# Performance work log

Measured on AMD Instinct MI355X. Metric: run time of the kernel, lower is better.

## Reference

```python
import jax, jax.numpy as jnp
import numpy as np

D_IN, D_H1, D_H2, D_OUT = 24, 64, 128, 64

def setup_inputs() -> dict:
    key = jax.random.key(0)
    ks = jax.random.split(key, 7)
    B, L = 256, 2048
    input_data = jax.random.normal(ks[0], (B, L, D_IN), dtype=jnp.float32)
    s = lambda fan_in: 1.0 / np.sqrt(fan_in)
    W1 = jax.random.uniform(ks[1], (D_IN, D_H1), minval=-s(D_IN), maxval=s(D_IN), dtype=jnp.float32)
    b1 = jax.random.uniform(ks[2], (D_H1,), minval=-s(D_IN), maxval=s(D_IN), dtype=jnp.float32)
    W2 = jax.random.uniform(ks[3], (D_H1, D_H2), minval=-s(D_H1), maxval=s(D_H1), dtype=jnp.float32)
    b2 = jax.random.uniform(ks[4], (D_H2,), minval=-s(D_H1), maxval=s(D_H1), dtype=jnp.float32)
    W3 = jax.random.uniform(ks[5], (D_H2, D_OUT), minval=-s(D_H2), maxval=s(D_H2), dtype=jnp.float32)
    b3 = jax.random.uniform(ks[6], (D_OUT,), minval=-s(D_H2), maxval=s(D_H2), dtype=jnp.float32)
    return {"input_data": input_data, "W1": W1, "b1": b1, "W2": W2, "b2": b2, "W3": W3, "b3": b3, "batch_size": 256}

def reference(input_data, W1, b1, W2, b2, W3, b3, batch_size):
    # Vectorized equivalent of the per-(batch,line) MLP loop:
    # three Linear+ReLU layers applied to every [24]-dim vector.
    h = jax.nn.relu(jnp.einsum('bli,ij->blj', input_data, W1) + b1)
    h = jax.nn.relu(jnp.einsum('bli,ij->blj', h, W2) + b2)
    out = jax.nn.relu(jnp.einsum('bli,ij->blj', h, W3) + b3)  # [B, L, 64]
    return out
```

## Files before the change

kernel.cpp:

```cpp
#include <hip/hip_runtime.h>

typedef float f32x4 __attribute__((ext_vector_type(4)));
typedef short s16x8 __attribute__((ext_vector_type(8)));

#define DIN 24
#define DH1 64
#define DH2 128
#define DOUT 64
#define H1PAD 80
#define H2PAD 136

static __device__ __forceinline__ unsigned short f2bf(float f) {
    unsigned int u = __builtin_bit_cast(unsigned int, f);
    u += 0x7FFFu + ((u >> 16) & 1u);
    return (unsigned short)(u >> 16);
}

__global__ __launch_bounds__(256, 2) void linenet_mfma(
    const float* __restrict__ in,
    const float* __restrict__ W1, const float* __restrict__ b1,
    const float* __restrict__ W2, const float* __restrict__ b2,
    const float* __restrict__ W3, const float* __restrict__ b3,
    float* __restrict__ out, int M)
{
    __shared__ __align__(16) unsigned short w3lds[16 * 64 * 8];
    __shared__ __align__(16) unsigned short h1lds[4][16 * H1PAD];
    __shared__ __align__(16) unsigned short h2lds[4][16 * H2PAD];

    const int tid = threadIdx.x;

    for (int it = tid; it < 16 * 64; it += 256) {
        const int frag = it >> 6;
        const int ln   = it & 63;
        const int ks   = frag >> 2, nt = frag & 3;
        const int g    = ln >> 4,   c  = ln & 15;
        #pragma unroll
        for (int j = 0; j < 8; ++j) {
            const int k = 32 * ks + 8 * g + j;
            w3lds[it * 8 + j] = f2bf(W3[k * DOUT + nt * 16 + c]);
        }
    }
    __syncthreads();

    const int wave = tid >> 6, lane = tid & 63;
    const int gl = lane >> 4, cl = lane & 15;

    s16x8 w1f[4];
    #pragma unroll
    for (int nt = 0; nt < 4; ++nt) {
        #pragma unroll
        for (int j = 0; j < 8; ++j) {
            const int k = 8 * gl + j;
            w1f[nt][j] = (k < DIN) ? (short)f2bf(W1[k * DH1 + nt * 16 + cl]) : (short)0;
        }
    }
    s16x8 w2f[2][8];
    #pragma unroll
    for (int ks = 0; ks < 2; ++ks)
        #pragma unroll
        for (int nt = 0; nt < 8; ++nt)
            #pragma unroll
            for (int j = 0; j < 8; ++j)
                w2f[ks][nt][j] = (short)f2bf(W2[(32 * ks + 8 * gl + j) * DH2 + nt * 16 + cl]);

    float b1v[4], b2v[8], b3v[4];
    #pragma unroll
    for (int nt = 0; nt < 4; ++nt) b1v[nt] = b1[nt * 16 + cl];
    #pragma unroll
    for (int nt = 0; nt < 8; ++nt) b2v[nt] = b2[nt * 16 + cl];
    #pragma unroll
    for (int nt = 0; nt < 4; ++nt) b3v[nt] = b3[nt * 16 + cl];

    unsigned short* const h1p = &h1lds[wave][0];
    unsigned short* const h2p = &h2lds[wave][0];

    const int NT = M / 16;
    const int nw = (int)gridDim.x * 4;
    int t = (int)blockIdx.x * 4 + wave;
    if (t >= NT) return;

    const int goff = (gl < 3) ? 8 * gl : 16;
    const int loff = cl * DIN + goff;

    f32x4 pf0, pf1;
    {
        const float* p = in + (size_t)t * (16 * DIN) + loff;
        pf0 = *(const f32x4*)p;
        pf1 = *(const f32x4*)(p + 4);
    }

    f32x4 zac = {0.f, 0.f, 0.f, 0.f};

    while (t < NT) {
        s16x8 a1;
        #pragma unroll
        for (int j = 0; j < 4; ++j) {
            a1[j]     = (short)f2bf(pf0[j]);
            a1[4 + j] = (short)f2bf(pf1[j]);
        }

        const int tn = t + nw;
        {
            const int tc = (tn < NT) ? tn : t;
            const float* p = in + (size_t)tc * (16 * DIN) + loff;
            pf0 = *(const f32x4*)p;
            pf1 = *(const f32x4*)(p + 4);
        }

        f32x4 acc1[4];
        #pragma unroll
        for (int nt = 0; nt < 4; ++nt)
            acc1[nt] = __builtin_amdgcn_mfma_f32_16x16x32_bf16(a1, w1f[nt], zac, 0, 0, 0);

        #pragma unroll
        for (int nt = 0; nt < 4; ++nt)
            #pragma unroll
            for (int r = 0; r < 4; ++r) {
                float v = fmaxf(acc1[nt][r] + b1v[nt], 0.f);
                h1p[(4 * gl + r) * H1PAD + nt * 16 + cl] = f2bf(v);
            }

        s16x8 a2[2];
        #pragma unroll
        for (int ks = 0; ks < 2; ++ks)
            a2[ks] = *(const s16x8*)&h1p[cl * H1PAD + 32 * ks + 8 * gl];

        f32x4 acc2[8];
        #pragma unroll
        for (int nt = 0; nt < 8; ++nt)
            acc2[nt] = __builtin_amdgcn_mfma_f32_16x16x32_bf16(a2[0], w2f[0][nt], zac, 0, 0, 0);
        #pragma unroll
        for (int nt = 0; nt < 8; ++nt)
            acc2[nt] = __builtin_amdgcn_mfma_f32_16x16x32_bf16(a2[1], w2f[1][nt], acc2[nt], 0, 0, 0);

        #pragma unroll
        for (int nt = 0; nt < 8; ++nt)
            #pragma unroll
            for (int r = 0; r < 4; ++r) {
                float v = fmaxf(acc2[nt][r] + b2v[nt], 0.f);
                h2p[(4 * gl + r) * H2PAD + nt * 16 + cl] = f2bf(v);
            }

        f32x4 acc3[4];
        #pragma unroll
        for (int ks = 0; ks < 4; ++ks) {
            const s16x8 a3 = *(const s16x8*)&h2p[cl * H2PAD + 32 * ks + 8 * gl];
            #pragma unroll
            for (int nt = 0; nt < 4; ++nt) {
                const s16x8 wf = *(const s16x8*)&w3lds[((ks * 4 + nt) * 64 + lane) * 8];
                acc3[nt] = __builtin_amdgcn_mfma_f32_16x16x32_bf16(
                    a3, wf, (ks == 0) ? zac : acc3[nt], 0, 0, 0);
            }
        }

        float* const ob = out + (size_t)t * (16 * DOUT);
        #pragma unroll
        for (int nt = 0; nt < 4; ++nt)
            #pragma unroll
            for (int r = 0; r < 4; ++r) {
                float v = fmaxf(acc3[nt][r] + b3v[nt], 0.f);
                ob[(4 * gl + r) * DOUT + nt * 16 + cl] = v;
            }

        t = tn;
    }
}

extern "C" void kernel_launch(void* const* d_in, const int* in_sizes, int n_in,
                              void* d_out, int out_size, void* d_ws, size_t ws_size,
                              hipStream_t stream)
{
    const float* in = (const float*)d_in[0];
    const float* W1 = (const float*)d_in[1];
    const float* b1 = (const float*)d_in[2];
    const float* W2 = (const float*)d_in[3];
    const float* b2 = (const float*)d_in[4];
    const float* W3 = (const float*)d_in[5];
    const float* b3 = (const float*)d_in[6];
    float* out = (float*)d_out;
    const int M = in_sizes[0] / DIN;

    dim3 grid(512), block(256);
    hipLaunchKernelGGL(linenet_mfma, grid, block, 0, stream,
                       in, W1, b1, W2, b2, W3, b3, out, M);
}
```

Baseline: 49.92 us.

## Transpose MFMA operands so outputs are row-contiguous, fold bias into layer one

Swaps the MFMA operand order so each lane's accumulator holds four consecutive output features of one row. This allows packed bf16 stores to LDS via v_cvt_pk_bf16_f32 and 16-byte vector global stores instead of scalar scattered writes. The layer-1 bias is folded into the matmul by placing a constant 1.0 in the padded K slot. W3 fragments now live in registers instead of LDS, which raises register pressure under the 2-wave-per-SIMD launch bound.

```diff
diff --git a/kernel.cpp b/kernel.cpp
--- a/kernel.cpp
+++ b/kernel.cpp
@@ -2,74 +2,76 @@
 
 typedef float f32x4 __attribute__((ext_vector_type(4)));
 typedef short s16x8 __attribute__((ext_vector_type(8)));
+typedef unsigned int u32;
 
 #define DIN 24
 #define DH1 64
 #define DH2 128
 #define DOUT 64
-#define H1PAD 80
-#define H2PAD 136
+#define S1 72
+#define S2 136
 
 static __device__ __forceinline__ unsigned short f2bf(float f) {
-    unsigned int u = __builtin_bit_cast(unsigned int, f);
+    u32 u = __builtin_bit_cast(u32, f);
     u += 0x7FFFu + ((u >> 16) & 1u);
     return (unsigned short)(u >> 16);
 }
 
-__global__ __launch_bounds__(256, 2) void linenet_mfma(
+static __device__ __forceinline__ u32 cvtpk(float lo, float hi) {
+    u32 r;
+    asm("v_cvt_pk_bf16_f32 %0, %1, %2" : "=v"(r) : "v"(lo), "v"(hi));
+    return r;
+}
+
+__global__ __launch_bounds__(256, 2) void linenet_mfma_t(
     const float* __restrict__ in,
     const float* __restrict__ W1, const float* __restrict__ b1,
     const float* __restrict__ W2, const float* __restrict__ b2,
     const float* __restrict__ W3, const float* __restrict__ b3,
     float* __restrict__ out, int M)
 {
-    __shared__ __align__(16) unsigned short w3lds[16 * 64 * 8];
-    __shared__ __align__(16) unsigned short h1lds[4][16 * H1PAD];
-    __shared__ __align__(16) unsigned short h2lds[4][16 * H2PAD];
+    __shared__ __align__(16) unsigned short h1lds[4][1152];
+    __shared__ __align__(16) unsigned short h2lds[4][2176];
 
-    const int tid = threadIdx.x;
-
-    for (int it = tid; it < 16 * 64; it += 256) {
-        const int frag = it >> 6;
-        const int ln   = it & 63;
-        const int ks   = frag >> 2, nt = frag & 3;
-        const int g    = ln >> 4,   c  = ln & 15;
-        #pragma unroll
-        for (int j = 0; j < 8; ++j) {
-            const int k = 32 * ks + 8 * g + j;
-            w3lds[it * 8 + j] = f2bf(W3[k * DOUT + nt * 16 + c]);
-        }
-    }
-    __syncthreads();
-
+    const int tid  = threadIdx.x;
     const int wave = tid >> 6, lane = tid & 63;
     const int gl = lane >> 4, cl = lane & 15;
 
-    s16x8 w1f[4];
+    s16x8 w1tf[4];
     #pragma unroll
-    for (int nt = 0; nt < 4; ++nt) {
+    for (int nt = 0; nt < 4; ++nt)
         #pragma unroll
         for (int j = 0; j < 8; ++j) {
             const int k = 8 * gl + j;
-            w1f[nt][j] = (k < DIN) ? (short)f2bf(W1[k * DH1 + nt * 16 + cl]) : (short)0;
+            unsigned short v = 0;
+            if (k < DIN)       v = f2bf(W1[k * DH1 + nt * 16 + cl]);
+            else if (k == DIN) v = f2bf(b1[nt * 16 + cl]);
+            w1tf[nt][j] = (short)v;
         }
-    }
-    s16x8 w2f[2][8];
+    s16x8 w2tf[8][2];
     #pragma unroll
-    for (int ks = 0; ks < 2; ++ks)
+    for (int mt = 0; mt < 8; ++mt)
         #pragma unroll
-        for (int nt = 0; nt < 8; ++nt)
+        for (int ks = 0; ks < 2; ++ks)
             #pragma unroll
             for (int j = 0; j < 8; ++j)
-                w2f[ks][nt][j] = (short)f2bf(W2[(32 * ks + 8 * gl + j) * DH2 + nt * 16 + cl]);
+                w2tf[mt][ks][j] =
+                    (short)f2bf(W2[(32 * ks + 8 * gl + j) * DH2 + mt * 16 + cl]);
+    s16x8 w3tf[4][4];
+    #pragma unroll
+    for (int nt = 0; nt < 4; ++nt)
+        #pragma unroll
+        for (int ks = 0; ks < 4; ++ks)
+            #pragma unroll
+            for (int j = 0; j < 8; ++j)
+                w3tf[nt][ks][j] =
+                    (short)f2bf(W3[(32 * ks + 8 * gl + j) * DOUT + nt * 16 + cl]);
 
-    float b1v[4], b2v[8], b3v[4];
+    f32x4 b2v4[8], b3v4[4];
     #pragma unroll
-    for (int nt = 0; nt < 4; ++nt) b1v[nt] = b1[nt * 16 + cl];
+    for (int mt = 0; mt < 8; ++mt) b2v4[mt] = *(const f32x4*)&b2[16 * mt + 4 * gl];
     #pragma unroll
-    for (int nt = 0; nt < 8; ++nt) b2v[nt] = b2[nt * 16 + cl];
-    #pragma unroll
-    for (int nt = 0; nt < 4; ++nt) b3v[nt] = b3[nt * 16 + cl];
+    for (int nt = 0; nt < 4; ++nt) b3v4[nt] = *(const f32x4*)&b3[16 * nt + 4 * gl];
 
     unsigned short* const h1p = &h1lds[wave][0];
     unsigned short* const h2p = &h2lds[wave][0];
@@ -79,7 +81,7 @@
     int t = (int)blockIdx.x * 4 + wave;
     if (t >= NT) return;
 
-    const int goff = (gl < 3) ? 8 * gl : 16;
+    const int goff = (gl < 3) ? 8 * gl : 0;
     const int loff = cl * DIN + goff;
 
     f32x4 pf0, pf1;
@@ -89,14 +91,20 @@
         pf1 = *(const f32x4*)(p + 4);
     }
 
-    f32x4 zac = {0.f, 0.f, 0.f, 0.f};
+    const f32x4 zac = {0.f, 0.f, 0.f, 0.f};
 
     while (t < NT) {
+        u32 a1w[4];
+        a1w[0] = cvtpk(pf0[0], pf0[1]);
+        a1w[1] = cvtpk(pf0[2], pf0[3]);
+        a1w[2] = cvtpk(pf1[0], pf1[1]);
+        a1w[3] = cvtpk(pf1[2], pf1[3]);
+        if (gl == 3) a1w[0] = 0x00003F80u;
         s16x8 a1;
         #pragma unroll
-        for (int j = 0; j < 4; ++j) {
-            a1[j]     = (short)f2bf(pf0[j]);
-            a1[4 + j] = (short)f2bf(pf1[j]);
+        for (int p = 0; p < 4; ++p) {
+            a1[2 * p]     = (short)(a1w[p] & 0xFFFFu);
+            a1[2 * p + 1] = (short)(a1w[p] >> 16);
         }
 
         const int tn = t + nw;
@@ -110,57 +118,57 @@
         f32x4 acc1[4];
         #pragma unroll
         for (int nt = 0; nt < 4; ++nt)
-            acc1[nt] = __builtin_amdgcn_mfma_f32_16x16x32_bf16(a1, w1f[nt], zac, 0, 0, 0);
+            acc1[nt] = __builtin_amdgcn_mfma_f32_16x16x32_bf16(w1tf[nt], a1, zac, 0, 0, 0);
 
         #pragma unroll
-        for (int nt = 0; nt < 4; ++nt)
-            #pragma unroll
-            for (int r = 0; r < 4; ++r) {
-                float v = fmaxf(acc1[nt][r] + b1v[nt], 0.f);
-                h1p[(4 * gl + r) * H1PAD + nt * 16 + cl] = f2bf(v);
-            }
+        for (int nt = 0; nt < 4; ++nt) {
+            const float v0 = fmaxf(acc1[nt][0], 0.f), v1 = fmaxf(acc1[nt][1], 0.f);
+            const float v2 = fmaxf(acc1[nt][2], 0.f), v3 = fmaxf(acc1[nt][3], 0.f);
+            u32* w = (u32*)&h1p[cl * S1 + 16 * nt + 4 * gl];
+            w[0] = cvtpk(v0, v1);
+            w[1] = cvtpk(v2, v3);
+        }
 
-        s16x8 a2[2];
-        #pragma unroll
-        for (int ks = 0; ks < 2; ++ks)
-            a2[ks] = *(const s16x8*)&h1p[cl * H1PAD + 32 * ks + 8 * gl];
-
+        s16x8 bh1[2];
+        bh1[0] = *(const s16x8*)&h1p[cl * S1 + 0  + 8 * gl];
+        bh1[1] = *(const s16x8*)&h1p[cl * S1 + 32 + 8 * gl];
         f32x4 acc2[8];
         #pragma unroll
-        for (int nt = 0; nt < 8; ++nt)
-            acc2[nt] = __builtin_amdgcn_mfma_f32_16x16x32_bf16(a2[0], w2f[0][nt], zac, 0, 0, 0);
+        for (int mt = 0; mt < 8; ++mt)
+            acc2[mt] = __builtin_amdgcn_mfma_f32_16x16x32_bf16(w2tf[mt][0], bh1[0], zac, 0, 0, 0);
         #pragma unroll
-        for (int nt = 0; nt < 8; ++nt)
-            acc2[nt] = __builtin_amdgcn_mfma_f32_16x16x32_bf16(a2[1], w2f[1][nt], acc2[nt], 0, 0, 0);
+        for (int mt = 0; mt < 8; ++mt)
+            acc2[mt] = __builtin_amdgcn_mfma_f32_16x16x32_bf16(w2tf[mt][1], bh1[1], acc2[mt], 0, 0, 0);
 
         #pragma unroll
-        for (int nt = 0; nt < 8; ++nt)
-            #pragma unroll
-            for (int r = 0; r < 4; ++r) {
-                float v = fmaxf(acc2[nt][r] + b2v[nt], 0.f);
-                h2p[(4 * gl + r) * H2PAD + nt * 16 + cl] = f2bf(v);
-            }
+        for (int mt = 0; mt < 8; ++mt) {
+            const f32x4 s = acc2[mt] + b2v4[mt];
+            const float v0 = fmaxf(s[0], 0.f), v1 = fmaxf(s[1], 0.f);
+            const float v2 = fmaxf(s[2], 0.f), v3 = fmaxf(s[3], 0.f);
+            u32* w = (u32*)&h2p[cl * S2 + 16 * mt + 4 * gl];
+            w[0] = cvtpk(v0, v1);
+            w[1] = cvtpk(v2, v3);
+        }
 
         f32x4 acc3[4];
         #pragma unroll
         for (int ks = 0; ks < 4; ++ks) {
-            const s16x8 a3 = *(const s16x8*)&h2p[cl * H2PAD + 32 * ks + 8 * gl];
+            const s16x8 bh2 = *(const s16x8*)&h2p[cl * S2 + 32 * ks + 8 * gl];
             #pragma unroll
-            for (int nt = 0; nt < 4; ++nt) {
-                const s16x8 wf = *(const s16x8*)&w3lds[((ks * 4 + nt) * 64 + lane) * 8];
+            for (int nt = 0; nt < 4; ++nt)
                 acc3[nt] = __builtin_amdgcn_mfma_f32_16x16x32_bf16(
-                    a3, wf, (ks == 0) ? zac : acc3[nt], 0, 0, 0);
-            }
+                    w3tf[nt][ks], bh2, (ks == 0) ? zac : acc3[nt], 0, 0, 0);
         }
 
-        float* const ob = out + (size_t)t * (16 * DOUT);
+        float* const ob = out + (size_t)t * (16 * DOUT) + (size_t)cl * DOUT;
         #pragma unroll
-        for (int nt = 0; nt < 4; ++nt)
-            #pragma unroll
-            for (int r = 0; r < 4; ++r) {
-                float v = fmaxf(acc3[nt][r] + b3v[nt], 0.f);
-                ob[(4 * gl + r) * DOUT + nt * 16 + cl] = v;
-            }
+        for (int nt = 0; nt < 4; ++nt) {
+            const f32x4 s = acc3[nt] + b3v4[nt];
+            f32x4 v;
+            v[0] = fmaxf(s[0], 0.f); v[1] = fmaxf(s[1], 0.f);
+            v[2] = fmaxf(s[2], 0.f); v[3] = fmaxf(s[3], 0.f);
+            *(f32x4*)&ob[16 * nt + 4 * gl] = v;
+        }
 
         t = tn;
     }
@@ -181,6 +189,6 @@
     const int M = in_sizes[0] / DIN;
 
     dim3 grid(512), block(256);
-    hipLaunchKernelGGL(linenet_mfma, grid, block, 0, stream,
+    hipLaunchKernelGGL(linenet_mfma_t, grid, block, 0, stream,
                        in, W1, b1, W2, b2, W3, b3, out, M);
 }
```

Result: faster. 43.85 us (-12.1%).
